# Performance work log

Measured on AMD Instinct MI355X. Metric: run time of the kernel, lower is better.

## Reference

```python
import jax, jax.numpy as jnp
import numpy as np

B, S, D = 2, 2048, 1024
H = 16
DK = D // H  # 64

def setup_inputs() -> dict:
    key = jax.random.key(0)
    ks = jax.random.split(key, 7)
    scale = 1.0 / np.sqrt(D)
    return {
        "Query": jax.random.normal(ks[0], (B, S, D), dtype=jnp.float32),
        "Key":   jax.random.normal(ks[1], (B, S, D), dtype=jnp.float32),
        "Value": jax.random.normal(ks[2], (B, S, D), dtype=jnp.float32),
        "Wq": jax.random.normal(ks[3], (D, D), dtype=jnp.float32) * scale,
        "Wk": jax.random.normal(ks[4], (D, D), dtype=jnp.float32) * scale,
        "Wv": jax.random.normal(ks[5], (D, D), dtype=jnp.float32) * scale,
        "Wo": jax.random.normal(ks[6], (D, D), dtype=jnp.float32) * scale,
    }

def reference(Query, Key, Value, Wq, Wk, Wv, Wo):
    b = Query.shape[0]
    # nn.Linear(bias=False): x @ W.T ; reshape to [B, H, S, DK]
    q = (Query @ Wq.T).reshape(b, -1, H, DK).transpose(0, 2, 1, 3)
    k = (Key   @ Wk.T).reshape(b, -1, H, DK).transpose(0, 2, 1, 3)
    v = (Value @ Wv.T).reshape(b, -1, H, DK).transpose(0, 2, 1, 3)
    # full O(S^2) score matrix [B, H, Sq, Sk]
    scores = jnp.einsum("bhqd,bhkd->bhqk", q, k) / jnp.sqrt(jnp.float32(DK))
    # FAITHFUL to source: nn.Softmax(dim=1) normalizes over the HEAD axis
    attn = jax.nn.softmax(scores, axis=1)
    ctx = jnp.einsum("bhqk,bhkd->bhqd", attn, v)  # [B, H, Sq, DK]
    ctx = ctx.transpose(0, 2, 1, 3).reshape(b, -1, H * DK)  # [B, S, D]
    return ctx @ Wo.T
```

## Files before the change

### kernel.cpp

```cpp
#include <hip/hip_runtime.h>
#include <stdint.h>

#define BB   2
#define SS   2048
#define DD   1024
#define HH   16
#define DKK  64
#define MM   (BB*SS)

typedef __attribute__((ext_vector_type(4))) float f32x4;
typedef __attribute__((ext_vector_type(8))) short s16x8;

union RdU { ushort u[8]; s16x8 v; };

#define MFMA_B16(a, b, c) __builtin_amdgcn_mfma_f32_16x16x32_bf16((a), (b), (c), 0, 0, 0)

__device__ __forceinline__ ushort f2bf(float f) {
  uint u = __float_as_uint(f);
  u += 0x7FFFu + ((u >> 16) & 1u);
  return (ushort)(u >> 16);
}
__device__ __forceinline__ float bf2f(ushort u) {
  return __uint_as_float((uint)u << 16);
}
#if __has_builtin(__builtin_amdgcn_exp2f)
#define EXP2(x) __builtin_amdgcn_exp2f(x)
#else
#define EXP2(x) exp2f(x)
#endif

__device__ __forceinline__ s16x8 pack8(float4 a, float4 b) {
  union { uint u[4]; s16x8 v; } r;
  asm("v_cvt_pk_bf16_f32 %0, %1, %2" : "=v"(r.u[0]) : "v"(a.x), "v"(a.y));
  asm("v_cvt_pk_bf16_f32 %0, %1, %2" : "=v"(r.u[1]) : "v"(a.z), "v"(a.w));
  asm("v_cvt_pk_bf16_f32 %0, %1, %2" : "=v"(r.u[2]) : "v"(b.x), "v"(b.y));
  asm("v_cvt_pk_bf16_f32 %0, %1, %2" : "=v"(r.u[3]) : "v"(b.z), "v"(b.w));
  return r.v;
}
__device__ __forceinline__ s16x8 cvt8(const float* src) {
  return pack8(*(const float4*)src, *(const float4*)(src + 4));
}

#define QSCALE (0.125f * 1.4426950408889634f)

__global__ void cvt4_kernel(const float* __restrict__ s0, const float* __restrict__ s1,
                            const float* __restrict__ s2, const float* __restrict__ s3,
                            ushort* __restrict__ d0, ushort* __restrict__ d1,
                            ushort* __restrict__ d2, ushort* __restrict__ d3, int n) {
  const int w = blockIdx.y;
  const float*  src = (w == 0) ? s0 : (w == 1) ? s1 : (w == 2) ? s2 : s3;
  ushort*       dst = (w == 0) ? d0 : (w == 1) ? d1 : (w == 2) ? d2 : d3;
  int i = (blockIdx.x * 256 + threadIdx.x) * 8;
  if (i >= n) return;
  *(s16x8*)(dst + i) = cvt8(src + i);
}

__global__ __launch_bounds__(256, 2) void qkv_proj(
    const float* __restrict__ Ia, const float* __restrict__ Ib, const float* __restrict__ Ic,
    const ushort* __restrict__ Wa, const ushort* __restrict__ Wb, const ushort* __restrict__ Wc,
    ushort* __restrict__ Oa, ushort* __restrict__ Ob, ushort* __restrict__ Oc)
{
  __shared__ ushort As[2][128 * 32];
  __shared__ ushort Bs[2][128 * 32];
  const int tid  = threadIdx.x;
  const int lane = tid & 63, wave = tid >> 6;
  const int q = lane & 15, g = lane >> 4;
  const int wr = wave >> 1, wc = wave & 1;
  const int mblk = blockIdx.x * 128, nblk = blockIdx.y * 128;
  const int mode = blockIdx.z;

  const float*  A = (mode == 0) ? Ia : (mode == 1) ? Ib : Ic;
  const ushort* W = (mode == 0) ? Wa : (mode == 1) ? Wb : Wc;

  f32x4 acc[4][4];
  {
    f32x4 z = {0.f, 0.f, 0.f, 0.f};
#pragma unroll
    for (int i = 0; i < 4; ++i)
#pragma unroll
      for (int j = 0; j < 4; ++j) acc[i][j] = z;
  }

  const int r0 = tid >> 2;
  const int e0 = (tid & 3) * 8;
  const size_t arow0 = (size_t)(mblk + r0) * 1024 + e0;
  const size_t arow1 = (size_t)(mblk + r0 + 64) * 1024 + e0;
  const size_t wrow0 = (size_t)(nblk + r0) * 1024 + e0;
  const size_t wrow1 = (size_t)(nblk + r0 + 64) * 1024 + e0;

#pragma unroll
  for (int it = 0; it < 2; ++it) {
    const int row = r0 + it * 64;
    *(s16x8*)&As[0][row * 32 + e0] = cvt8(A + (it ? arow1 : arow0));
    *(s16x8*)&Bs[0][row * 32 + e0] = *(const s16x8*)(W + (it ? wrow1 : wrow0));
  }
  float4 fa0_0, fa0_1, fa1_0, fa1_1;
  s16x8  wg0, wg1;
  {
    const float* p0 = A + arow0 + 32;
    const float* p1 = A + arow1 + 32;
    fa0_0 = *(const float4*)p0;  fa0_1 = *(const float4*)(p0 + 4);
    fa1_0 = *(const float4*)p1;  fa1_1 = *(const float4*)(p1 + 4);
    wg0 = *(const s16x8*)(W + wrow0 + 32);
    wg1 = *(const s16x8*)(W + wrow1 + 32);
  }
  __syncthreads();

  for (int s = 0; s < 32; ++s) {
    const int cur = s & 1;
    float4 na0_0, na0_1, na1_0, na1_1;
    s16x8  nw0, nw1;
    if (s < 30) {
      const int k0 = (s + 2) * 32;
      const float* p0 = A + arow0 + k0;
      const float* p1 = A + arow1 + k0;
      na0_0 = *(const float4*)p0;  na0_1 = *(const float4*)(p0 + 4);
      na1_0 = *(const float4*)p1;  na1_1 = *(const float4*)(p1 + 4);
      nw0 = *(const s16x8*)(W + wrow0 + k0);
      nw1 = *(const s16x8*)(W + wrow1 + k0);
    }
    s16x8 af[4], bf[4];
#pragma unroll
    for (int t = 0; t < 4; ++t) {
      af[t] = *(const s16x8*)&As[cur][(wr * 64 + t * 16 + q) * 32 + g * 8];
      bf[t] = *(const s16x8*)&Bs[cur][(wc * 64 + t * 16 + q) * 32 + g * 8];
    }
#pragma unroll
    for (int mt = 0; mt < 4; ++mt)
#pragma unroll
      for (int nt = 0; nt < 4; ++nt)
        acc[mt][nt] = MFMA_B16(af[mt], bf[nt], acc[mt][nt]);
    if (s < 31) {
      *(s16x8*)&As[cur ^ 1][r0 * 32 + e0]        = pack8(fa0_0, fa0_1);
      *(s16x8*)&As[cur ^ 1][(r0 + 64) * 32 + e0] = pack8(fa1_0, fa1_1);
      *(s16x8*)&Bs[cur ^ 1][r0 * 32 + e0]        = wg0;
      *(s16x8*)&Bs[cur ^ 1][(r0 + 64) * 32 + e0] = wg1;
    }
    if (s < 30) {
      fa0_0 = na0_0; fa0_1 = na0_1; fa1_0 = na1_0; fa1_1 = na1_1;
      wg0 = nw0; wg1 = nw1;
    }
    __syncthreads();
  }

  if (mode == 2) {
    ushort* Vt = Oc;
#pragma unroll
    for (int mt = 0; mt < 4; ++mt)
#pragma unroll
      for (int nt = 0; nt < 4; ++nt) {
        const int s0 = mblk + wr * 64 + mt * 16 + g * 4;
        const int o  = nblk + wc * 64 + nt * 16 + q;
        const int h = o >> 6, dk = o & 63;
        const int b = s0 >> 11, sr = s0 & 2047;
        ushort4 pk;
        pk.x = f2bf(acc[mt][nt][0]); pk.y = f2bf(acc[mt][nt][1]);
        pk.z = f2bf(acc[mt][nt][2]); pk.w = f2bf(acc[mt][nt][3]);
        *(ushort4*)(Vt + ((size_t)((b * 16 + h) * 64 + dk)) * SS + sr) = pk;
      }
  } else {
    const float scale = (mode == 0) ? QSCALE : 1.0f;
    ushort* P = (mode == 0) ? Oa : Ob;
    ushort* wl = &As[0][wave * 1024];
    const int h0 = (nblk + wc * 64) >> 6;
#pragma unroll
    for (int mt = 0; mt < 4; ++mt) {
      const int s0 = mblk + wr * 64 + mt * 16;
      const int b  = s0 >> 11, sr0 = s0 & 2047;
#pragma unroll
      for (int nt = 0; nt < 4; ++nt)
#pragma unroll
        for (int j = 0; j < 4; ++j)
          wl[(g * 4 + j) * 64 + nt * 16 + q] = f2bf(acc[mt][nt][j] * scale);
#pragma unroll
      for (int it = 0; it < 2; ++it) {
        s16x8 v = *(const s16x8*)((char*)wl + it * 1024 + lane * 16);
        const int lr = it * 8 + (lane >> 3);
        const int c  = (lane & 7) * 8;
        *(s16x8*)(P + ((size_t)((b * 16 + h0) * SS) + sr0 + lr) * DKK + c) = v;
      }
    }
  }
}

__global__ __launch_bounds__(256, 2) void o_proj(
    const ushort* __restrict__ A, const ushort* __restrict__ W,
    float* __restrict__ O)
{
  __shared__ ushort As[2][128 * 32];
  __shared__ ushort Bs[2][128 * 32];
  const int tid  = threadIdx.x;
  const int lane = tid & 63, wave = tid >> 6;
  const int q = lane & 15, g = lane >> 4;
  const int wr = wave >> 1, wc = wave & 1;
  const int mblk = blockIdx.x * 128, nblk = blockIdx.y * 128;

  f32x4 acc[4][4];
  {
    f32x4 z = {0.f, 0.f, 0.f, 0.f};
#pragma unroll
    for (int i = 0; i < 4; ++i)
#pragma unroll
      for (int j = 0; j < 4; ++j) acc[i][j] = z;
  }

  const int r0 = tid >> 2;
  const int e0 = (tid & 3) * 8;
  const size_t arow0 = (size_t)(mblk + r0) * 1024 + e0;
  const size_t arow1 = (size_t)(mblk + r0 + 64) * 1024 + e0;
  const size_t wrow0 = (size_t)(nblk + r0) * 1024 + e0;
  const size_t wrow1 = (size_t)(nblk + r0 + 64) * 1024 + e0;

#pragma unroll
  for (int it = 0; it < 2; ++it) {
    const int row = r0 + it * 64;
    *(s16x8*)&As[0][row * 32 + e0] = *(const s16x8*)(A + (it ? arow1 : arow0));
    *(s16x8*)&Bs[0][row * 32 + e0] = *(const s16x8*)(W + (it ? wrow1 : wrow0));
  }
  s16x8 ag0, ag1, wg0, wg1;
  {
    ag0 = *(const s16x8*)(A + arow0 + 32);
    ag1 = *(const s16x8*)(A + arow1 + 32);
    wg0 = *(const s16x8*)(W + wrow0 + 32);
    wg1 = *(const s16x8*)(W + wrow1 + 32);
  }
  __syncthreads();

  for (int s = 0; s < 32; ++s) {
    const int cur = s & 1;
    s16x8 na0, na1, nw0, nw1;
    if (s < 30) {
      const int k0 = (s + 2) * 32;
      na0 = *(const s16x8*)(A + arow0 + k0);
      na1 = *(const s16x8*)(A + arow1 + k0);
      nw0 = *(const s16x8*)(W + wrow0 + k0);
      nw1 = *(const s16x8*)(W + wrow1 + k0);
    }
    s16x8 af[4], bf[4];
#pragma unroll
    for (int t = 0; t < 4; ++t) {
      af[t] = *(const s16x8*)&As[cur][(wr * 64 + t * 16 + q) * 32 + g * 8];
      bf[t] = *(const s16x8*)&Bs[cur][(wc * 64 + t * 16 + q) * 32 + g * 8];
    }
#pragma unroll
    for (int mt = 0; mt < 4; ++mt)
#pragma unroll
      for (int nt = 0; nt < 4; ++nt)
        acc[mt][nt] = MFMA_B16(af[mt], bf[nt], acc[mt][nt]);
    if (s < 31) {
      *(s16x8*)&As[cur ^ 1][r0 * 32 + e0]        = ag0;
      *(s16x8*)&As[cur ^ 1][(r0 + 64) * 32 + e0] = ag1;
      *(s16x8*)&Bs[cur ^ 1][r0 * 32 + e0]        = wg0;
      *(s16x8*)&Bs[cur ^ 1][(r0 + 64) * 32 + e0] = wg1;
    }
    if (s < 30) { ag0 = na0; ag1 = na1; wg0 = nw0; wg1 = nw1; }
    __syncthreads();
  }

#pragma unroll
  for (int mt = 0; mt < 4; ++mt)
#pragma unroll
    for (int nt = 0; nt < 4; ++nt)
#pragma unroll
      for (int j = 0; j < 4; ++j) {
        const int s = mblk + wr * 64 + mt * 16 + g * 4 + j;
        const int o = nblk + wc * 64 + nt * 16 + q;
        O[(size_t)s * DD + o] = acc[mt][nt][j];
      }
}

__global__ __launch_bounds__(256, 2) void den_kernel(
    const ushort* __restrict__ Qp, const ushort* __restrict__ Kp,
    ushort* __restrict__ Rden)
{
  __shared__ ushort smem[2][16384];
  const int tid  = threadIdx.x;
  const int lane = tid & 63, wave = tid >> 6;
  const int q = lane & 15, g = lane >> 4;
  const int wr = wave >> 1, wc = wave & 1;
  const int kblk = blockIdx.x * 128, qblk = blockIdx.y * 128;
  const int b = blockIdx.z;

  f32x4 den[4][4];
  {
    f32x4 z = {0.f, 0.f, 0.f, 0.f};
#pragma unroll
    for (int i = 0; i < 4; ++i)
#pragma unroll
      for (int j = 0; j < 4; ++j) den[i][j] = z;
  }

  const int srow = tid >> 3, sseg = tid & 7;
  const int sd   = (sseg * 8) ^ ((srow & 7) << 3);

  const ushort* Kb0 = Kp + ((size_t)(b * 16) * SS + kblk) * DKK;
  const ushort* Qb0 = Qp + ((size_t)(b * 16) * SS + qblk) * DKK;

#pragma unroll
  for (int i = 0; i < 4; ++i) {
    const int row = srow + i * 32;
    *(s16x8*)&smem[0][row * 64 + sd]        = *(const s16x8*)(Kb0 + (size_t)row * DKK + sseg * 8);
    *(s16x8*)&smem[0][8192 + row * 64 + sd] = *(const s16x8*)(Qb0 + (size_t)row * DKK + sseg * 8);
  }
  __syncthreads();

  for (int s = 0; s < 16; ++s) {
    const int cur = s & 1;
    s16x8 nA[4], nB[4];
    if (s < 15) {
      const ushort* Kh = Kb0 + (size_t)(s + 1) * SS * DKK;
      const ushort* Qh = Qb0 + (size_t)(s + 1) * SS * DKK;
#pragma unroll
      for (int i = 0; i < 4; ++i) {
        const int row = srow + i * 32;
        nA[i] = *(const s16x8*)(Kh + (size_t)row * DKK + sseg * 8);
        nB[i] = *(const s16x8*)(Qh + (size_t)row * DKK + sseg * 8);
      }
    }
    s16x8 af[4][2], bf[4][2];
#pragma unroll
    for (int t = 0; t < 4; ++t) {
      const int ra = wr * 64 + t * 16 + q;
      const int rb = wc * 64 + t * 16 + q;
      af[t][0] = *(const s16x8*)&smem[cur][ra * 64 + ((g * 8) ^ ((ra & 7) << 3))];
      af[t][1] = *(const s16x8*)&smem[cur][ra * 64 + ((32 + g * 8) ^ ((ra & 7) << 3))];
      bf[t][0] = *(const s16x8*)&smem[cur][8192 + rb * 64 + ((g * 8) ^ ((rb & 7) << 3))];
      bf[t][1] = *(const s16x8*)&smem[cur][8192 + rb * 64 + ((32 + g * 8) ^ ((rb & 7) << 3))];
    }
#pragma unroll
    for (int mt = 0; mt < 4; ++mt)
#pragma unroll
      for (int nt = 0; nt < 4; ++nt) {
        f32x4 c = {0.f, 0.f, 0.f, 0.f};
        c = MFMA_B16(af[mt][0], bf[nt][0], c);
        c = MFMA_B16(af[mt][1], bf[nt][1], c);
#pragma unroll
        for (int r = 0; r < 4; ++r)
          den[mt][nt][r] += EXP2(c[r]);
      }
    if (s < 15) {
#pragma unroll
      for (int i = 0; i < 4; ++i) {
        const int row = srow + i * 32;
        *(s16x8*)&smem[cur ^ 1][row * 64 + sd]        = nA[i];
        *(s16x8*)&smem[cur ^ 1][8192 + row * 64 + sd] = nB[i];
      }
    }
    __syncthreads();
  }

  ushort* R2 = Rden + (((size_t)(b * 16 + blockIdx.y) * 32) + (blockIdx.x * 2 + wr)) * 8192;
#pragma unroll
  for (int nt = 0; nt < 4; ++nt) {
    const int tid_t = (wc * 4 + nt) * 64 + g * 16 + q;
#pragma unroll
    for (int mt = 0; mt < 4; ++mt) {
      const float i0 = 1.0f / den[mt][nt][0], i1 = 1.0f / den[mt][nt][1];
      const float i2 = 1.0f / den[mt][nt][2], i3 = 1.0f / den[mt][nt][3];
      union { ushort4 s; uint2 u; } pk;
      asm("v_cvt_pk_bf16_f32 %0, %1, %2" : "=v"(pk.u.x) : "v"(i0), "v"(i1));
      asm("v_cvt_pk_bf16_f32 %0, %1, %2" : "=v"(pk.u.y) : "v"(i2), "v"(i3));
      *(ushort4*)(R2 + tid_t * 16 + mt * 4) = pk.s;
    }
  }
}

__global__ __launch_bounds__(512, 2) void attn5_kernel(
    const ushort* __restrict__ Qp, const ushort* __restrict__ Kp,
    const ushort* __restrict__ Vt, const ushort* __restrict__ Rden,
    ushort* __restrict__ Ctx)
{
  __shared__ ushort Ktile[2][64 * 64];
  __shared__ ushort Vtile[2][64 * 64];
  __shared__ ushort aw_all[8][16 * 64];

  const int tid  = threadIdx.x;
  const int lane = tid & 63;
  const int w    = tid >> 6;
  const int q    = lane & 15;
  const int g    = lane >> 4;
  const int bid  = blockIdx.x;
  const int bh   = bid & 31;
  const int b    = bh >> 4, h = bh & 15;
  const int qt   = bid >> 5;
  const int qblk = qt * 128;

  const ushort* Qb = Qp + ((size_t)bh * SS + qblk + w * 16 + q) * DKK + g * 8;
  s16x8 qf0 = *(const s16x8*)(Qb);
  s16x8 qf1 = *(const s16x8*)(Qb + 32);

  const ushort* Ks = Kp + (size_t)bh * SS * DKK;
  const ushort* Vs = Vt + (size_t)bh * DKK * SS;
  const ushort* Rs = Rden + ((size_t)(b * 16 + qt) * 32) * 8192 + tid * 16;

  f32x4 acc[4];
  {
    f32x4 z = {0.f, 0.f, 0.f, 0.f};
#pragma unroll
    for (int n = 0; n < 4; ++n) acc[n] = z;
  }

  ushort* aw = aw_all[w];
  const int srow = tid >> 3, sseg = tid & 7;
  const int sd   = (sseg * 8) ^ ((srow & 7) << 3);

  RdU rdA, rdB;
  {
    s16x8 gK  = *(const s16x8*)(Ks + tid * 8);
    s16x8 gV  = *(const s16x8*)(Vs + (size_t)srow * SS + sseg * 8);
    rdA.v = *(const s16x8*)(Rs);
    rdB.v = *(const s16x8*)(Rs + 8);
    *(s16x8*)&Ktile[0][srow * 64 + sd] = gK;
    *(s16x8*)&Vtile[0][srow * 64 + sd] = gV;
  }
  __syncthreads();

  for (int kt = 0; kt < 32; ++kt) {
    const int cur = kt & 1;
    s16x8 gK, gV;
    RdU nrA, nrB;
    if (kt < 31) {
      const int k1 = (kt + 1) * 64;
      gK  = *(const s16x8*)(Ks + (size_t)k1 * DKK + tid * 8);
      gV  = *(const s16x8*)(Vs + (size_t)srow * SS + k1 + sseg * 8);
      nrA.v = *(const s16x8*)(Rs + (size_t)(kt + 1) * 8192);
      nrB.v = *(const s16x8*)(Rs + (size_t)(kt + 1) * 8192 + 8);
    }
    const ushort* Kt = Ktile[cur];
    const ushort* Vv = Vtile[cur];

#pragma unroll
    for (int ks = 0; ks < 4; ++ks) {
      const int kr = ks * 16 + q;
      s16x8 a0 = *(const s16x8*)&Kt[kr * 64 + ((g * 8) ^ ((kr & 7) << 3))];
      s16x8 a1 = *(const s16x8*)&Kt[kr * 64 + ((32 + g * 8) ^ ((kr & 7) << 3))];
      f32x4 c = {0.f, 0.f, 0.f, 0.f};
      c = MFMA_B16(a0, qf0, c);
      c = MFMA_B16(a1, qf1, c);
      const ushort* ru = (ks < 2) ? rdA.u : rdB.u;
      const int o4 = (ks & 1) * 4;
      float p0 = EXP2(c[0]) * bf2f(ru[o4 + 0]);
      float p1 = EXP2(c[1]) * bf2f(ru[o4 + 1]);
      float p2 = EXP2(c[2]) * bf2f(ru[o4 + 2]);
      float p3 = EXP2(c[3]) * bf2f(ru[o4 + 3]);
      uint2 pp;
      asm("v_cvt_pk_bf16_f32 %0, %1, %2" : "=v"(pp.x) : "v"(p0), "v"(p1));
      asm("v_cvt_pk_bf16_f32 %0, %1, %2" : "=v"(pp.y) : "v"(p2), "v"(p3));
      *(uint2*)&aw[q * 64 + ((ks * 16 + g * 4) ^ ((q & 7) << 3))] = pp;
    }
#pragma unroll
    for (int kc = 0; kc < 2; ++kc) {
      s16x8 vf[4];
#pragma unroll
      for (int n = 0; n < 4; ++n) {
        const int vr = n * 16 + q;
        vf[n] = *(const s16x8*)&Vv[vr * 64 + ((kc * 32 + g * 8) ^ ((vr & 7) << 3))];
      }
      s16x8 pa = *(const s16x8*)&aw[q * 64 + ((kc * 32 + g * 8) ^ ((q & 7) << 3))];
#pragma unroll
      for (int n = 0; n < 4; ++n)
        acc[n] = MFMA_B16(pa, vf[n], acc[n]);
    }
    if (kt < 31) {
      *(s16x8*)&Ktile[cur ^ 1][srow * 64 + sd] = gK;
      *(s16x8*)&Vtile[cur ^ 1][srow * 64 + sd] = gV;
      rdA = nrA; rdB = nrB;
    }
    __syncthreads();
  }

#pragma unroll
  for (int n = 0; n < 4; ++n)
#pragma unroll
    for (int j = 0; j < 4; ++j)
      aw[(g * 4 + j) * 64 + n * 16 + q] = f2bf(acc[n][j]);
  ushort* P = Ctx + ((size_t)(b * SS) + qblk + w * 16) * DD + h * 64;
#pragma unroll
  for (int it = 0; it < 2; ++it) {
    const int idx = it * 64 + lane;
    const int row = idx >> 3;
    const int seg = idx & 7;
    s16x8 v = *(const s16x8*)&aw[row * 64 + seg * 8];
    *(s16x8*)(P + (size_t)row * DD + seg * 8) = v;
  }
}

extern "C" void kernel_launch(void* const* d_in, const int* in_sizes, int n_in,
                              void* d_out, int out_size, void* d_ws, size_t ws_size,
                              hipStream_t stream) {
  const float* Query = (const float*)d_in[0];
  const float* Key   = (const float*)d_in[1];
  const float* Value = (const float*)d_in[2];
  const float* Wq    = (const float*)d_in[3];
  const float* Wk    = (const float*)d_in[4];
  const float* Wv    = (const float*)d_in[5];
  const float* Wo    = (const float*)d_in[6];

  size_t off = 0;
  char* ws = (char*)d_ws;
  auto alloc = [&](size_t bytes) -> void* {
    void* p = ws + off;
    off += (bytes + 255) & ~(size_t)255;
    return p;
  };
  const size_t nX = (size_t)MM * DD;
  const size_t nW = (size_t)DD * DD;
  const size_t nS = (size_t)BB * SS * SS;
  ushort* Wqb  = (ushort*)alloc(nW * 2);
  ushort* Wkb  = (ushort*)alloc(nW * 2);
  ushort* Wvb  = (ushort*)alloc(nW * 2);
  ushort* Wob  = (ushort*)alloc(nW * 2);
  ushort* Qp   = (ushort*)alloc(nX * 2);
  ushort* Kp   = (ushort*)alloc(nX * 2);
  ushort* Vtb  = (ushort*)alloc(nX * 2);
  ushort* Rden = (ushort*)alloc(nS * 2);
  ushort* Ctx  = (ushort*)alloc(nX * 2);

  cvt4_kernel<<<dim3((int)(nW / 2048), 4), 256, 0, stream>>>(
      Wq, Wk, Wv, Wo, Wqb, Wkb, Wvb, Wob, (int)nW);

  qkv_proj<<<dim3(32, 8, 3), 256, 0, stream>>>(
      Query, Key, Value, Wqb, Wkb, Wvb, Qp, Kp, Vtb);

  den_kernel<<<dim3(16, 16, 2), 256, 0, stream>>>(Qp, Kp, Rden);
  attn5_kernel<<<512, 512, 0, stream>>>(Qp, Kp, Vtb, Rden, Ctx);

  o_proj<<<dim3(32, 8), 256, 0, stream>>>(Ctx, Wob, (float*)d_out);
}
```

Before: 143.6 us.

## Double K-tile depth to 64 with XOR-swizzled LDS in projection GEMMs

Both the QKV projection and the output projection GEMMs now stage 64-wide K tiles instead of 32, which halves the main-loop iterations and barriers. The LDS layout applies an XOR swizzle on 8-element segments to avoid bank conflicts on the wider rows. The prefetch distance drops from two tiles ahead to one, and LDS use doubles to 64KB per block, which may limit occupancy alongside the launch bounds.

```diff
diff --git a/kernel.cpp b/kernel.cpp
--- a/kernel.cpp
+++ b/kernel.cpp
@@ -60,8 +60,8 @@
     const ushort* __restrict__ Wa, const ushort* __restrict__ Wb, const ushort* __restrict__ Wc,
     ushort* __restrict__ Oa, ushort* __restrict__ Ob, ushort* __restrict__ Oc)
 {
-  __shared__ ushort As[2][128 * 32];
-  __shared__ ushort Bs[2][128 * 32];
+  __shared__ ushort As[2][128 * 64];
+  __shared__ ushort Bs[2][128 * 64];
   const int tid  = threadIdx.x;
   const int lane = tid & 63, wave = tid >> 6;
   const int q = lane & 15, g = lane >> 4;
@@ -81,64 +81,56 @@
       for (int j = 0; j < 4; ++j) acc[i][j] = z;
   }
 
-  const int r0 = tid >> 2;
-  const int e0 = (tid & 3) * 8;
-  const size_t arow0 = (size_t)(mblk + r0) * 1024 + e0;
-  const size_t arow1 = (size_t)(mblk + r0 + 64) * 1024 + e0;
-  const size_t wrow0 = (size_t)(nblk + r0) * 1024 + e0;
-  const size_t wrow1 = (size_t)(nblk + r0 + 64) * 1024 + e0;
-
-#pragma unroll
-  for (int it = 0; it < 2; ++it) {
-    const int row = r0 + it * 64;
-    *(s16x8*)&As[0][row * 32 + e0] = cvt8(A + (it ? arow1 : arow0));
-    *(s16x8*)&Bs[0][row * 32 + e0] = *(const s16x8*)(W + (it ? wrow1 : wrow0));
-  }
-  float4 fa0_0, fa0_1, fa1_0, fa1_1;
-  s16x8  wg0, wg1;
-  {
-    const float* p0 = A + arow0 + 32;
-    const float* p1 = A + arow1 + 32;
-    fa0_0 = *(const float4*)p0;  fa0_1 = *(const float4*)(p0 + 4);
-    fa1_0 = *(const float4*)p1;  fa1_1 = *(const float4*)(p1 + 4);
-    wg0 = *(const s16x8*)(W + wrow0 + 32);
-    wg1 = *(const s16x8*)(W + wrow1 + 32);
+  const int srow = tid >> 3, sseg = tid & 7;
+  const int sd   = (sseg * 8) ^ ((srow & 7) << 3);
+
+#pragma unroll
+  for (int i = 0; i < 4; ++i) {
+    const int row = srow + i * 32;
+    *(s16x8*)&As[0][row * 64 + sd] = cvt8(A + (size_t)(mblk + row) * 1024 + sseg * 8);
+    *(s16x8*)&Bs[0][row * 64 + sd] = *(const s16x8*)(W + (size_t)(nblk + row) * 1024 + sseg * 8);
   }
   __syncthreads();
 
-  for (int s = 0; s < 32; ++s) {
+  for (int s = 0; s < 16; ++s) {
     const int cur = s & 1;
-    float4 na0_0, na0_1, na1_0, na1_1;
-    s16x8  nw0, nw1;
-    if (s < 30) {
-      const int k0 = (s + 2) * 32;
-      const float* p0 = A + arow0 + k0;
-      const float* p1 = A + arow1 + k0;
-      na0_0 = *(const float4*)p0;  na0_1 = *(const float4*)(p0 + 4);
-      na1_0 = *(const float4*)p1;  na1_1 = *(const float4*)(p1 + 4);
-      nw0 = *(const s16x8*)(W + wrow0 + k0);
-      nw1 = *(const s16x8*)(W + wrow1 + k0);
-    }
-    s16x8 af[4], bf[4];
+    float4 nfa[4][2];
+    s16x8  nw[4];
+    if (s < 15) {
+      const int k0 = (s + 1) * 64;
+#pragma unroll
+      for (int i = 0; i < 4; ++i) {
+        const int row = srow + i * 32;
+        const float* pa = A + (size_t)(mblk + row) * 1024 + k0 + sseg * 8;
+        nfa[i][0] = *(const float4*)pa;
+        nfa[i][1] = *(const float4*)(pa + 4);
+        nw[i] = *(const s16x8*)(W + (size_t)(nblk + row) * 1024 + k0 + sseg * 8);
+      }
+    }
+    s16x8 af[4][2], bf[4][2];
 #pragma unroll
     for (int t = 0; t < 4; ++t) {
-      af[t] = *(const s16x8*)&As[cur][(wr * 64 + t * 16 + q) * 32 + g * 8];
-      bf[t] = *(const s16x8*)&Bs[cur][(wc * 64 + t * 16 + q) * 32 + g * 8];
+      const int ra = wr * 64 + t * 16 + q;
+      const int rb = wc * 64 + t * 16 + q;
+      af[t][0] = *(const s16x8*)&As[cur][ra * 64 + ((g * 8) ^ ((ra & 7) << 3))];
+      af[t][1] = *(const s16x8*)&As[cur][ra * 64 + ((32 + g * 8) ^ ((ra & 7) << 3))];
+      bf[t][0] = *(const s16x8*)&Bs[cur][rb * 64 + ((g * 8) ^ ((rb & 7) << 3))];
+      bf[t][1] = *(const s16x8*)&Bs[cur][rb * 64 + ((32 + g * 8) ^ ((rb & 7) << 3))];
     }
 #pragma unroll
     for (int mt = 0; mt < 4; ++mt)
 #pragma unroll
-      for (int nt = 0; nt < 4; ++nt)
-        acc[mt][nt] = MFMA_B16(af[mt], bf[nt], acc[mt][nt]);
-    if (s < 31) {
-      *(s16x8*)&As[cur ^ 1][r0 * 32 + e0]        = pack8(fa0_0, fa0_1);
-      *(s16x8*)&As[cur ^ 1][(r0 + 64) * 32 + e0] = pack8(fa1_0, fa1_1);
-      *(s16x8*)&Bs[cur ^ 1][r0 * 32 + e0]        = wg0;
-      *(s16x8*)&Bs[cur ^ 1][(r0 + 64) * 32 + e0] = wg1;
-    }
-    if (s < 30) {
-      fa0_0 = na0_0; fa0_1 = na0_1; fa1_0 = na1_0; fa1_1 = na1_1;
-      wg0 = nw0; wg1 = nw1;
+      for (int nt = 0; nt < 4; ++nt) {
+        acc[mt][nt] = MFMA_B16(af[mt][0], bf[nt][0], acc[mt][nt]);
+        acc[mt][nt] = MFMA_B16(af[mt][1], bf[nt][1], acc[mt][nt]);
+      }
+    if (s < 15) {
+#pragma unroll
+      for (int i = 0; i < 4; ++i) {
+        const int row = srow + i * 32;
+        *(s16x8*)&As[cur ^ 1][row * 64 + sd] = pack8(nfa[i][0], nfa[i][1]);
+        *(s16x8*)&Bs[cur ^ 1][row * 64 + sd] = nw[i];
+      }
     }
     __syncthreads();
   }
@@ -187,8 +179,8 @@
     const ushort* __restrict__ A, const ushort* __restrict__ W,
     float* __restrict__ O)
 {
-  __shared__ ushort As[2][128 * 32];
-  __shared__ ushort Bs[2][128 * 32];
+  __shared__ ushort As[2][128 * 64];
+  __shared__ ushort Bs[2][128 * 64];
   const int tid  = threadIdx.x;
   const int lane = tid & 63, wave = tid >> 6;
   const int q = lane & 15, g = lane >> 4;
@@ -204,56 +196,54 @@
       for (int j = 0; j < 4; ++j) acc[i][j] = z;
   }
 
-  const int r0 = tid >> 2;
-  const int e0 = (tid & 3) * 8;
-  const size_t arow0 = (size_t)(mblk + r0) * 1024 + e0;
-  const size_t arow1 = (size_t)(mblk + r0 + 64) * 1024 + e0;
-  const size_t wrow0 = (size_t)(nblk + r0) * 1024 + e0;
-  const size_t wrow1 = (size_t)(nblk + r0 + 64) * 1024 + e0;
-
-#pragma unroll
-  for (int it = 0; it < 2; ++it) {
-    const int row = r0 + it * 64;
-    *(s16x8*)&As[0][row * 32 + e0] = *(const s16x8*)(A + (it ? arow1 : arow0));
-    *(s16x8*)&Bs[0][row * 32 + e0] = *(const s16x8*)(W + (it ? wrow1 : wrow0));
-  }
-  s16x8 ag0, ag1, wg0, wg1;
-  {
-    ag0 = *(const s16x8*)(A + arow0 + 32);
-    ag1 = *(const s16x8*)(A + arow1 + 32);
-    wg0 = *(const s16x8*)(W + wrow0 + 32);
-    wg1 = *(const s16x8*)(W + wrow1 + 32);
+  const int srow = tid >> 3, sseg = tid & 7;
+  const int sd   = (sseg * 8) ^ ((srow & 7) << 3);
+
+#pragma unroll
+  for (int i = 0; i < 4; ++i) {
+    const int row = srow + i * 32;
+    *(s16x8*)&As[0][row * 64 + sd] = *(const s16x8*)(A + (size_t)(mblk + row) * 1024 + sseg * 8);
+    *(s16x8*)&Bs[0][row * 64 + sd] = *(const s16x8*)(W + (size_t)(nblk + row) * 1024 + sseg * 8);
   }
   __syncthreads();
 
-  for (int s = 0; s < 32; ++s) {
+  for (int s = 0; s < 16; ++s) {
     const int cur = s & 1;
-    s16x8 na0, na1, nw0, nw1;
-    if (s < 30) {
-      const int k0 = (s + 2) * 32;
-      na0 = *(const s16x8*)(A + arow0 + k0);
-      na1 = *(const s16x8*)(A + arow1 + k0);
-      nw0 = *(const s16x8*)(W + wrow0 + k0);
-      nw1 = *(const s16x8*)(W + wrow1 + k0);
-    }
-    s16x8 af[4], bf[4];
+    s16x8 nA[4], nW2[4];
+    if (s < 15) {
+      const int k0 = (s + 1) * 64;
+#pragma unroll
+      for (int i = 0; i < 4; ++i) {
+        const int row = srow + i * 32;
+        nA[i]  = *(const s16x8*)(A + (size_t)(mblk + row) * 1024 + k0 + sseg * 8);
+        nW2[i] = *(const s16x8*)(W + (size_t)(nblk + row) * 1024 + k0 + sseg * 8);
+      }
+    }
+    s16x8 af[4][2], bf[4][2];
 #pragma unroll
     for (int t = 0; t < 4; ++t) {
-      af[t] = *(const s16x8*)&As[cur][(wr * 64 + t * 16 + q) * 32 + g * 8];
-      bf[t] = *(const s16x8*)&Bs[cur][(wc * 64 + t * 16 + q) * 32 + g * 8];
+      const int ra = wr * 64 + t * 16 + q;
+      const int rb = wc * 64 + t * 16 + q;
+      af[t][0] = *(const s16x8*)&As[cur][ra * 64 + ((g * 8) ^ ((ra & 7) << 3))];
+      af[t][1] = *(const s16x8*)&As[cur][ra * 64 + ((32 + g * 8) ^ ((ra & 7) << 3))];
+      bf[t][0] = *(const s16x8*)&Bs[cur][rb * 64 + ((g * 8) ^ ((rb & 7) << 3))];
+      bf[t][1] = *(const s16x8*)&Bs[cur][rb * 64 + ((32 + g * 8) ^ ((rb & 7) << 3))];
     }
 #pragma unroll
     for (int mt = 0; mt < 4; ++mt)
 #pragma unroll
-      for (int nt = 0; nt < 4; ++nt)
-        acc[mt][nt] = MFMA_B16(af[mt], bf[nt], acc[mt][nt]);
-    if (s < 31) {
-      *(s16x8*)&As[cur ^ 1][r0 * 32 + e0]        = ag0;
-      *(s16x8*)&As[cur ^ 1][(r0 + 64) * 32 + e0] = ag1;
-      *(s16x8*)&Bs[cur ^ 1][r0 * 32 + e0]        = wg0;
-      *(s16x8*)&Bs[cur ^ 1][(r0 + 64) * 32 + e0] = wg1;
-    }
-    if (s < 30) { ag0 = na0; ag1 = na1; wg0 = nw0; wg1 = nw1; }
+      for (int nt = 0; nt < 4; ++nt) {
+        acc[mt][nt] = MFMA_B16(af[mt][0], bf[nt][0], acc[mt][nt]);
+        acc[mt][nt] = MFMA_B16(af[mt][1], bf[nt][1], acc[mt][nt]);
+      }
+    if (s < 15) {
+#pragma unroll
+      for (int i = 0; i < 4; ++i) {
+        const int row = srow + i * 32;
+        *(s16x8*)&As[cur ^ 1][row * 64 + sd] = nA[i];
+        *(s16x8*)&Bs[cur ^ 1][row * 64 + sd] = nW2[i];
+      }
+    }
     __syncthreads();
   }
 
```

Result: slower. 152.7 us (+6.4%).
